# Kernel optimization log

Measured on AMD Instinct MI355X. Metric: run time of the kernel, lower is better.

## Reference

```python
import jax, jax.numpy as jnp
import numpy as np

K, S, P, NQ, NREPS = 3, 1, 1, 9, 2  # kernel, stride, pad, num_qubits, num_qreps


def _extract_patches(x, k, s):
    # x: (b, c, H, W) -> (b, c, ho, wo, k*k), patch elems in (kh, kw) row-major order
    b, c, H, W = x.shape
    ho = (H - k) // s + 1
    wo = (W - k) // s + 1
    cols = [x[:, :, i:i + (ho - 1) * s + 1:s, j:j + (wo - 1) * s + 1:s]
            for i in range(k) for j in range(k)]
    return jnp.stack(cols, axis=-1), ho, wo


def _cnot(state, c, t):
    # state: (N, 2, ..., 2); CNOT with control wire c, target wire t (wire q -> axis q+1)
    s0, s1 = jnp.split(state, 2, axis=c + 1)
    return jnp.concatenate([s0, jnp.flip(s1, axis=t + 1)], axis=c + 1)


def _simulate(angles, weights):
    # AngleEmbedding(RX) + BasicEntanglerLayers(RZ, CNOT ring) + expval(PauliY_i)
    # angles: (N, n) float; weights: (L, n) float -> (N, n) float expvals
    N, n = angles.shape
    half = 0.5 * angles
    # RX(theta)|0> = cos(t/2)|0> - i sin(t/2)|1>  (product state)
    vecs = jnp.stack([jnp.cos(half).astype(jnp.complex64),
                      -1j * jnp.sin(half)], axis=-1)  # (N, n, 2)
    state = vecs[:, 0]
    for q in range(1, n):
        state = state[..., None] * vecs[:, q].reshape((N,) + (1,) * q + (2,))
    # state: (N, 2, ..., 2), wire 0 = axis 1 (most significant)
    for l in range(weights.shape[0]):
        # RZ layer = single diagonal of shape (2,)*n, shared across patches
        pv = jnp.stack([jnp.exp(-0.5j * weights[l]),
                        jnp.exp(0.5j * weights[l])], axis=-1).astype(jnp.complex64)  # (n,2)
        diag = pv[0]
        for q in range(1, n):
            diag = diag[..., None] * pv[q].reshape((1,) * q + (2,))
        state = state * diag
        # CNOT ring (i -> i+1 mod n), as in BasicEntanglerLayers for n > 2
        for i in range(n):
            state = _cnot(state, i, (i + 1) % n)
    # <Y_i> = 2 * Im( sum conj(psi_{qi=0}) * psi_{qi=1} )
    exps = []
    for i in range(n):
        a, bdim = 1 << i, 1 << (n - 1 - i)
        r = state.reshape(N, a, 2, bdim)
        z = jnp.sum(jnp.conj(r[:, :, 0, :]) * r[:, :, 1, :], axis=(1, 2))
        exps.append(2.0 * z.imag)
    return jnp.stack(exps, axis=1)  # (N, n) float32


def setup_inputs() -> dict:
    key = jax.random.key(0)
    k1, k2 = jax.random.split(key)
    x = jax.random.uniform(k1, (16, 1, 28, 28), dtype=jnp.float32)
    weights = jax.random.uniform(k2, (NREPS, NQ), dtype=jnp.float32,
                                 minval=0.0, maxval=2.0 * np.pi)
    return {"x": x, "weights": weights}


def reference(x, weights):
    b = x.shape[0]
    xp = jnp.pad(x, ((0, 0), (0, 0), (P, P), (P, P)))
    patches, ho, wo = _extract_patches(xp, K, S)  # (b, 1, ho, wo, k*k)
    flat = patches.reshape(-1, NQ)                # (b*ho*wo, 9)  (c == 1)
    qout = _simulate(flat, weights)               # (b*ho*wo, 9)
    qout = qout.reshape(b, ho, wo, NQ)
    return qout.transpose(0, 3, 1, 2)             # (b, 9, ho, wo)
```

## Files before the change

### kernel.cpp

```cpp
#include <hip/hip_runtime.h>
#include <math.h>

#define NQ 9
#define NREPS 2
#define NB 512
#define NSIMS (16*28*28)

__host__ __device__ constexpr int csigma(int b) {
    for (int c = NQ - 1; c >= 0; --c) {
        const int t  = (c + 1) % NQ;
        const int pc = NQ - 1 - c;
        const int pt = NQ - 1 - t;
        b ^= ((b >> pc) & 1) << pt;
    }
    return b;
}
__host__ __device__ constexpr int csig2(int b) { return csigma(csigma(b)); }

constexpr int VB_[6] = { csig2(1<<0), csig2(1<<1), csig2(1<<2),
                         csig2(1<<3), csig2(1<<4), csig2(1<<5) };
constexpr int VR_[8] = { csig2(0<<6), csig2(1<<6), csig2(2<<6), csig2(3<<6),
                         csig2(4<<6), csig2(5<<6), csig2(6<<6), csig2(7<<6) };

__device__ float2 g_T[NB];

__global__ void quanv_setup(const float* __restrict__ w) {
    const int b = threadIdx.x;
    if (b >= NB) return;
    float th = 0.f;
    int cur = b;
    #pragma unroll
    for (int l = NREPS - 1; l >= 0; --l) {
        cur = csigma(cur);
        #pragma unroll
        for (int q = 0; q < NQ; ++q) {
            const float wq = 0.5f * w[l * NQ + q];
            th += ((cur >> (NQ - 1 - q)) & 1) ? wq : -wq;
        }
    }
    th -= 1.5707963267948966f * (float)__popc((unsigned)cur);
    g_T[b] = make_float2(cosf(th), sinf(th));
}

template<int CTRL>
__device__ __forceinline__ float dppmov(float x) {
    return __int_as_float(__builtin_amdgcn_update_dpp(
        0, __float_as_int(x), CTRL, 0xF, 0xF, true));
}
template<int OFF>
__device__ __forceinline__ float swzx(float x) {
    return __int_as_float(__builtin_amdgcn_ds_swizzle(__float_as_int(x), OFF));
}
template<int P>
__device__ __forceinline__ float lane_xor(float x) {
    if constexpr (P == 0) return dppmov<0xB1>(x);
    else if constexpr (P == 1) return dppmov<0x4E>(x);
    else if constexpr (P == 2) return swzx<0x101F>(x);
    else if constexpr (P == 3) return dppmov<0x128>(x);
    else if constexpr (P == 4) return swzx<0x401F>(x);
    else return __shfl_xor(x, 32, 64);
}
__device__ __forceinline__ float wave_reduce(float v) {
    v += dppmov<0x111>(v);
    v += dppmov<0x112>(v);
    v += dppmov<0x114>(v);
    v += dppmov<0x118>(v);
    v += dppmov<0x142>(v);
    v += dppmov<0x143>(v);
    return v;
}

__global__ __launch_bounds__(256) void quanv_main(
    const float* __restrict__ x,
    float* __restrict__ out)
{
    const int tid  = blockIdx.x * blockDim.x + threadIdx.x;
    const int lane = threadIdx.x & 63;
    const int sim  = tid >> 6;
    const int ox  = sim % 28;
    const int oy  = (sim / 28) % 28;
    const int img = sim / 784;

    float cq[NQ], sq[NQ];
    #pragma unroll
    for (int q = 0; q < NQ; ++q) {
        const int ky = q / 3, kx = q % 3;
        const int y  = oy + ky - 1;
        const int xx = ox + kx - 1;
        float a = 0.f;
        if (y >= 0 && y < 28 && xx >= 0 && xx < 28)
            a = x[img * 784 + y * 28 + xx];
        __sincosf(0.5f * a, &sq[q], &cq[q]);
    }

    const int VL = ((lane & 1)  ? VB_[0] : 0) ^ ((lane & 2)  ? VB_[1] : 0)
                 ^ ((lane & 4)  ? VB_[2] : 0) ^ ((lane & 8)  ? VB_[3] : 0)
                 ^ ((lane & 16) ? VB_[4] : 0) ^ ((lane & 32) ? VB_[5] : 0);

    float P0[NQ], P1[NQ];
    #pragma unroll
    for (int q = 0; q < NQ; ++q) {
        const bool bit = (VL >> (NQ - 1 - q)) & 1;
        P0[q] = bit ? sq[q] : cq[q];
        P1[q] = bit ? cq[q] : sq[q];
    }

    float fre[8], fim[8];
    #pragma unroll
    for (int r = 0; r < 8; ++r) {
        float m = ((VR_[r] >> (NQ - 1)) & 1) ? P1[0] : P0[0];
        #pragma unroll
        for (int q = 1; q < NQ; ++q)
            m *= ((VR_[r] >> (NQ - 1 - q)) & 1) ? P1[q] : P0[q];
        const float2 T = g_T[(r << 6) | lane];
        fre[r] = m * T.x;
        fim[r] = m * T.y;
    }

    float e[NQ];
#define EXP_QUBIT(i, P)                                            \
    {                                                              \
        const float sign = ((lane >> (P)) & 1) ? -1.f : 1.f;       \
        float acc = 0.f;                                           \
        _Pragma("unroll")                                          \
        for (int r = 0; r < 8; ++r) {                              \
            const float gre = lane_xor<P>(fre[r]);                 \
            const float gim = lane_xor<P>(fim[r]);                 \
            acc += fre[r] * gim - fim[r] * gre;                    \
        }                                                          \
        e[i] = sign * acc;                                         \
    }
    EXP_QUBIT(8, 0)
    EXP_QUBIT(7, 1)
    EXP_QUBIT(6, 2)
    EXP_QUBIT(5, 3)
    EXP_QUBIT(4, 4)
    EXP_QUBIT(3, 5)
#undef EXP_QUBIT

    #pragma unroll
    for (int i = 0; i < 3; ++i) {
        const int rb = (NQ - 1 - i) - 6;
        float acc = 0.f;
        #pragma unroll
        for (int r = 0; r < 8; ++r) {
            if (!((r >> rb) & 1)) {
                const int r1 = r | (1 << rb);
                acc += fre[r] * fim[r1] - fim[r] * fre[r1];
            }
        }
        e[i] = 2.f * acc;
    }

    #pragma unroll
    for (int i = 0; i < NQ; ++i)
        e[i] = wave_reduce(e[i]);

    if (lane == 63) {
        float* o = out + img * (NQ * 784) + oy * 28 + ox;
        #pragma unroll
        for (int i = 0; i < NQ; ++i)
            o[i * 784] = e[i];
    }
}

extern "C" void kernel_launch(void* const* d_in, const int* in_sizes, int n_in,
                              void* d_out, int out_size, void* d_ws, size_t ws_size,
                              hipStream_t stream) {
    const float* x = (const float*)d_in[0];
    const float* w = (const float*)d_in[1];
    float* out = (float*)d_out;
    (void)d_ws; (void)ws_size; (void)in_sizes; (void)n_in; (void)out_size;

    quanv_setup<<<1, NB, 0, stream>>>(w);
    quanv_main<<<NSIMS / 4, 256, 0, stream>>>(x, out);
}
```

Baseline: 67.58 us.

## Use real-amplitude algebra with precomputed phase-difference sine tables for expectations

The state amplitudes are factored into a real product magnitude times a phase. Each Y-expectation then reduces to a sum of products of real magnitudes weighted by the sine of phase differences, which the setup kernel precomputes per qubit in a [qubit][lane][row] table. The main kernel now shuffles one real value per row instead of two, and replaces the complex cross-products with single FMAs. In exchange it reads a larger per-qubit table from global memory, nine float4 pairs per lane. The fused sincos is also split into separate fast sin and cos calls.

```diff
diff --git a/kernel.cpp b/kernel.cpp
--- a/kernel.cpp
+++ b/kernel.cpp
@@ -22,24 +22,35 @@
 constexpr int VR_[8] = { csig2(0<<6), csig2(1<<6), csig2(2<<6), csig2(3<<6),
                          csig2(4<<6), csig2(5<<6), csig2(6<<6), csig2(7<<6) };
 
-__device__ float2 g_T[NB];
+__device__ float g_Bt[NQ][64][8];
 
 __global__ void quanv_setup(const float* __restrict__ w) {
+    __shared__ float Th[NB];
     const int b = threadIdx.x;
-    if (b >= NB) return;
-    float th = 0.f;
-    int cur = b;
-    #pragma unroll
-    for (int l = NREPS - 1; l >= 0; --l) {
-        cur = csigma(cur);
+    if (b < NB) {
+        float th = 0.f;
+        int cur = b;
         #pragma unroll
-        for (int q = 0; q < NQ; ++q) {
-            const float wq = 0.5f * w[l * NQ + q];
-            th += ((cur >> (NQ - 1 - q)) & 1) ? wq : -wq;
+        for (int l = NREPS - 1; l >= 0; --l) {
+            cur = csigma(cur);
+            #pragma unroll
+            for (int q = 0; q < NQ; ++q) {
+                const float wq = 0.5f * w[l * NQ + q];
+                th += ((cur >> (NQ - 1 - q)) & 1) ? wq : -wq;
+            }
+        }
+        th -= 1.5707963267948966f * (float)__popc((unsigned)cur);
+        Th[b] = th;
+    }
+    __syncthreads();
+    if (b < NB) {
+        #pragma unroll
+        for (int i = 0; i < NQ; ++i) {
+            const int m = 1 << (NQ - 1 - i);
+            const float d = Th[b | m] - Th[b & ~m];
+            g_Bt[i][b & 63][b >> 6] = sinf(d);
         }
     }
-    th -= 1.5707963267948966f * (float)__popc((unsigned)cur);
-    g_T[b] = make_float2(cosf(th), sinf(th));
 }
 
 template<int CTRL>
@@ -90,7 +101,9 @@
         float a = 0.f;
         if (y >= 0 && y < 28 && xx >= 0 && xx < 28)
             a = x[img * 784 + y * 28 + xx];
-        __sincosf(0.5f * a, &sq[q], &cq[q]);
+        const float h = 0.5f * a;
+        sq[q] = __sinf(h);
+        cq[q] = __cosf(h);
     }
 
     const int VL = ((lane & 1)  ? VB_[0] : 0) ^ ((lane & 2)  ? VB_[1] : 0)
@@ -105,51 +118,52 @@
         P1[q] = bit ? cq[q] : sq[q];
     }
 
-    float fre[8], fim[8];
+    float m[8];
     #pragma unroll
     for (int r = 0; r < 8; ++r) {
-        float m = ((VR_[r] >> (NQ - 1)) & 1) ? P1[0] : P0[0];
+        float p = ((VR_[r] >> (NQ - 1)) & 1) ? P1[0] : P0[0];
         #pragma unroll
         for (int q = 1; q < NQ; ++q)
-            m *= ((VR_[r] >> (NQ - 1 - q)) & 1) ? P1[q] : P0[q];
-        const float2 T = g_T[(r << 6) | lane];
-        fre[r] = m * T.x;
-        fim[r] = m * T.y;
+            p *= ((VR_[r] >> (NQ - 1 - q)) & 1) ? P1[q] : P0[q];
+        m[r] = p;
     }
 
     float e[NQ];
-#define EXP_QUBIT(i, P)                                            \
-    {                                                              \
-        const float sign = ((lane >> (P)) & 1) ? -1.f : 1.f;       \
-        float acc = 0.f;                                           \
-        _Pragma("unroll")                                          \
-        for (int r = 0; r < 8; ++r) {                              \
-            const float gre = lane_xor<P>(fre[r]);                 \
-            const float gim = lane_xor<P>(fim[r]);                 \
-            acc += fre[r] * gim - fim[r] * gre;                    \
-        }                                                          \
-        e[i] = sign * acc;                                         \
+
+#define EXPQ(i, P)                                                   \
+    {                                                                \
+        const float4 blo = *(const float4*)(&g_Bt[i][lane][0]);      \
+        const float4 bhi = *(const float4*)(&g_Bt[i][lane][4]);      \
+        const float B_[8] = { blo.x, blo.y, blo.z, blo.w,            \
+                              bhi.x, bhi.y, bhi.z, bhi.w };          \
+        float acc = 0.f;                                             \
+        _Pragma("unroll")                                            \
+        for (int r = 0; r < 8; ++r) {                                \
+            const float gm = lane_xor<P>(m[r]);                      \
+            acc = fmaf(m[r] * gm, B_[r], acc);                       \
+        }                                                            \
+        e[i] = acc;                                                  \
     }
-    EXP_QUBIT(8, 0)
-    EXP_QUBIT(7, 1)
-    EXP_QUBIT(6, 2)
-    EXP_QUBIT(5, 3)
-    EXP_QUBIT(4, 4)
-    EXP_QUBIT(3, 5)
-#undef EXP_QUBIT
+    EXPQ(8, 0)
+    EXPQ(7, 1)
+    EXPQ(6, 2)
+    EXPQ(5, 3)
+    EXPQ(4, 4)
+    EXPQ(3, 5)
+#undef EXPQ
 
     #pragma unroll
     for (int i = 0; i < 3; ++i) {
-        const int rb = (NQ - 1 - i) - 6;
+        const int rb = 2 - i;
+        const float4 blo = *(const float4*)(&g_Bt[i][lane][0]);
+        const float4 bhi = *(const float4*)(&g_Bt[i][lane][4]);
+        const float B_[8] = { blo.x, blo.y, blo.z, blo.w,
+                              bhi.x, bhi.y, bhi.z, bhi.w };
         float acc = 0.f;
         #pragma unroll
-        for (int r = 0; r < 8; ++r) {
-            if (!((r >> rb) & 1)) {
-                const int r1 = r | (1 << rb);
-                acc += fre[r] * fim[r1] - fim[r] * fre[r1];
-            }
-        }
-        e[i] = 2.f * acc;
+        for (int r = 0; r < 8; ++r)
+            acc = fmaf(m[r] * m[r ^ (1 << rb)], B_[r], acc);
+        e[i] = acc;
     }
 
     #pragma unroll
```

Measured after the change: 70.30 us. 1.04x slower.

## Fuse phase-table setup into main kernel and pack swizzle exchanges as fp16

Applied to the files above, without the earlier changes.

Removes the separate setup launch: every block recomputes the 512-entry phase table into shared memory before its simulation work, which drops one kernel launch and the global-memory table. The LDS-based lane exchanges (ds_swizzle and the xor-32 shuffle) now move one packed half2 word instead of two floats, halving those permute operations. The input sincos is split into separate fast sin and cos calls. The costs are redundant table computation in every block with a precise sincosf, and reduced precision on the exchanged amplitudes.

```diff
diff --git a/kernel.cpp b/kernel.cpp
--- a/kernel.cpp
+++ b/kernel.cpp
@@ -22,43 +22,14 @@
 constexpr int VR_[8] = { csig2(0<<6), csig2(1<<6), csig2(2<<6), csig2(3<<6),
                          csig2(4<<6), csig2(5<<6), csig2(6<<6), csig2(7<<6) };
 
-__device__ float2 g_T[NB];
-
-__global__ void quanv_setup(const float* __restrict__ w) {
-    const int b = threadIdx.x;
-    if (b >= NB) return;
-    float th = 0.f;
-    int cur = b;
-    #pragma unroll
-    for (int l = NREPS - 1; l >= 0; --l) {
-        cur = csigma(cur);
-        #pragma unroll
-        for (int q = 0; q < NQ; ++q) {
-            const float wq = 0.5f * w[l * NQ + q];
-            th += ((cur >> (NQ - 1 - q)) & 1) ? wq : -wq;
-        }
-    }
-    th -= 1.5707963267948966f * (float)__popc((unsigned)cur);
-    g_T[b] = make_float2(cosf(th), sinf(th));
-}
-
 template<int CTRL>
 __device__ __forceinline__ float dppmov(float x) {
     return __int_as_float(__builtin_amdgcn_update_dpp(
         0, __float_as_int(x), CTRL, 0xF, 0xF, true));
 }
 template<int OFF>
-__device__ __forceinline__ float swzx(float x) {
-    return __int_as_float(__builtin_amdgcn_ds_swizzle(__float_as_int(x), OFF));
-}
-template<int P>
-__device__ __forceinline__ float lane_xor(float x) {
-    if constexpr (P == 0) return dppmov<0xB1>(x);
-    else if constexpr (P == 1) return dppmov<0x4E>(x);
-    else if constexpr (P == 2) return swzx<0x101F>(x);
-    else if constexpr (P == 3) return dppmov<0x128>(x);
-    else if constexpr (P == 4) return swzx<0x401F>(x);
-    else return __shfl_xor(x, 32, 64);
+__device__ __forceinline__ int swzx_i(int x) {
+    return __builtin_amdgcn_ds_swizzle(x, OFF);
 }
 __device__ __forceinline__ float wave_reduce(float v) {
     v += dppmov<0x111>(v);
@@ -70,10 +41,45 @@
     return v;
 }
 
-__global__ __launch_bounds__(256) void quanv_main(
+typedef __fp16 h2_t __attribute__((ext_vector_type(2)));
+__device__ __forceinline__ int packf16(float a, float b) {
+    h2_t h = __builtin_amdgcn_cvt_pkrtz(a, b);
+    int i; __builtin_memcpy(&i, &h, 4); return i;
+}
+__device__ __forceinline__ float2 unpackf16(int i) {
+    h2_t h; __builtin_memcpy(&h, &i, 4);
+    return make_float2((float)h.x, (float)h.y);
+}
+
+__global__ __launch_bounds__(256) void quanv_fused(
     const float* __restrict__ x,
+    const float* __restrict__ w,
     float* __restrict__ out)
 {
+    __shared__ float2 T[NB];
+    {
+        const int t = threadIdx.x;
+        #pragma unroll
+        for (int bb = t; bb < NB; bb += 256) {
+            float th = 0.f;
+            int cur = bb;
+            #pragma unroll
+            for (int l = NREPS - 1; l >= 0; --l) {
+                cur = csigma(cur);
+                #pragma unroll
+                for (int q = 0; q < NQ; ++q) {
+                    const float wq = 0.5f * w[l * NQ + q];
+                    th += ((cur >> (NQ - 1 - q)) & 1) ? wq : -wq;
+                }
+            }
+            th -= 1.5707963267948966f * (float)__popc((unsigned)cur);
+            float s, c;
+            sincosf(th, &s, &c);
+            T[bb] = make_float2(c, s);
+        }
+    }
+    __syncthreads();
+
     const int tid  = blockIdx.x * blockDim.x + threadIdx.x;
     const int lane = threadIdx.x & 63;
     const int sim  = tid >> 6;
@@ -90,7 +96,9 @@
         float a = 0.f;
         if (y >= 0 && y < 28 && xx >= 0 && xx < 28)
             a = x[img * 784 + y * 28 + xx];
-        __sincosf(0.5f * a, &sq[q], &cq[q]);
+        const float h = 0.5f * a;
+        sq[q] = __sinf(h);
+        cq[q] = __cosf(h);
     }
 
     const int VL = ((lane & 1)  ? VB_[0] : 0) ^ ((lane & 2)  ? VB_[1] : 0)
@@ -106,41 +114,67 @@
     }
 
     float fre[8], fim[8];
+    int   pk[8];
     #pragma unroll
     for (int r = 0; r < 8; ++r) {
         float m = ((VR_[r] >> (NQ - 1)) & 1) ? P1[0] : P0[0];
         #pragma unroll
         for (int q = 1; q < NQ; ++q)
             m *= ((VR_[r] >> (NQ - 1 - q)) & 1) ? P1[q] : P0[q];
-        const float2 T = g_T[(r << 6) | lane];
-        fre[r] = m * T.x;
-        fim[r] = m * T.y;
+        const float2 t = T[(r << 6) | lane];
+        fre[r] = m * t.x;
+        fim[r] = m * t.y;
+        pk[r]  = packf16(fre[r], fim[r]);
     }
 
     float e[NQ];
-#define EXP_QUBIT(i, P)                                            \
+
+#define EXPQ_DPP(i, P, CTRL)                                       \
     {                                                              \
         const float sign = ((lane >> (P)) & 1) ? -1.f : 1.f;       \
         float acc = 0.f;                                           \
         _Pragma("unroll")                                          \
         for (int r = 0; r < 8; ++r) {                              \
-            const float gre = lane_xor<P>(fre[r]);                 \
-            const float gim = lane_xor<P>(fim[r]);                 \
+            const float gre = dppmov<CTRL>(fre[r]);                \
+            const float gim = dppmov<CTRL>(fim[r]);                \
             acc += fre[r] * gim - fim[r] * gre;                    \
         }                                                          \
         e[i] = sign * acc;                                         \
     }
-    EXP_QUBIT(8, 0)
-    EXP_QUBIT(7, 1)
-    EXP_QUBIT(6, 2)
-    EXP_QUBIT(5, 3)
-    EXP_QUBIT(4, 4)
-    EXP_QUBIT(3, 5)
-#undef EXP_QUBIT
+    EXPQ_DPP(8, 0, 0xB1)
+    EXPQ_DPP(7, 1, 0x4E)
+    EXPQ_DPP(5, 3, 0x128)
+#undef EXPQ_DPP
+
+#define EXPQ_SWZ(i, P, OFF)                                        \
+    {                                                              \
+        const float sign = ((lane >> (P)) & 1) ? -1.f : 1.f;       \
+        float acc = 0.f;                                           \
+        _Pragma("unroll")                                          \
+        for (int r = 0; r < 8; ++r) {                              \
+            const float2 g = unpackf16(swzx_i<OFF>(pk[r]));        \
+            acc += fre[r] * g.y - fim[r] * g.x;                    \
+        }                                                          \
+        e[i] = sign * acc;                                         \
+    }
+    EXPQ_SWZ(6, 2, 0x101F)
+    EXPQ_SWZ(4, 4, 0x401F)
+#undef EXPQ_SWZ
+
+    {
+        const float sign = ((lane >> 5) & 1) ? -1.f : 1.f;
+        float acc = 0.f;
+        #pragma unroll
+        for (int r = 0; r < 8; ++r) {
+            const float2 g = unpackf16(__shfl_xor(pk[r], 32, 64));
+            acc += fre[r] * g.y - fim[r] * g.x;
+        }
+        e[3] = sign * acc;
+    }
 
     #pragma unroll
     for (int i = 0; i < 3; ++i) {
-        const int rb = (NQ - 1 - i) - 6;
+        const int rb = 2 - i;
         float acc = 0.f;
         #pragma unroll
         for (int r = 0; r < 8; ++r) {
@@ -172,6 +206,5 @@
     float* out = (float*)d_out;
     (void)d_ws; (void)ws_size; (void)in_sizes; (void)n_in; (void)out_size;
 
-    quanv_setup<<<1, NB, 0, stream>>>(w);
-    quanv_main<<<NSIMS / 4, 256, 0, stream>>>(x, out);
-}
+    quanv_fused<<<NSIMS / 4, 256, 0, stream>>>(x, w, out);
+}
```

After: 69.26 us. 1.02x slower.
